# Kernel optimization log

Hardware: AMD Instinct MI355X
Metric: run time of the kernel (lower is better)

Reference implementation:

```python
import jax, jax.numpy as jnp
import numpy as np

E = 8        # num_experts
K = 2        # experts_per_token
D = 1024     # embed_dim
F = 4096     # expert intermediate (mlp_ratio * D)
FS = 2048    # shared-expert intermediate (n_shared_experts * D)
B, S = 2, 1024


def setup_inputs() -> dict:
    key = jax.random.key(0)
    ks = jax.random.split(key, 8)
    scale = jnp.float32(0.02)
    return {
        "x": jax.random.normal(ks[0], (B, S, D), jnp.float32),
        "gate_w": jax.random.normal(ks[1], (E, D), jnp.float32) * scale,
        "gate_k": jax.random.normal(ks[2], (E, D, F), jnp.float32) * scale,
        "up_k": jax.random.normal(ks[3], (E, D, F), jnp.float32) * scale,
        "down_k": jax.random.normal(ks[4], (E, F, D), jnp.float32) * scale,
        "sh_gate": jax.random.normal(ks[5], (D, FS), jnp.float32) * scale,
        "sh_up": jax.random.normal(ks[6], (D, FS), jnp.float32) * scale,
        "sh_down": jax.random.normal(ks[7], (FS, D), jnp.float32) * scale,
    }


def reference(x, gate_w, gate_k, up_k, down_k, sh_gate, sh_up, sh_down):
    b, s, d = x.shape
    xt = x.reshape(-1, d)                                   # [N, D] tokens

    # --- router gate: softmax over expert logits, then top-k ---
    logits = xt @ gate_w.T                                  # [N, E]
    scores = jax.nn.softmax(logits, axis=-1)
    topk_w, topk_i = jax.lax.top_k(scores, K)               # [N, K] each
    # norm_topk_prob = False -> use raw softmax top-k weights

    # per-token combine weights over experts: [N, E]
    combine = (jax.nn.one_hot(topk_i, E, dtype=xt.dtype) * topk_w[..., None]).sum(axis=1)

    # --- routed experts: SwiGLU MLP per expert (batched over E) ---
    g = jnp.einsum("nd,edf->enf", xt, gate_k)               # [E, N, F]
    u = jnp.einsum("nd,edf->enf", xt, up_k)                 # [E, N, F]
    a = jax.nn.silu(g) * u                                  # [E, N, F]
    eo = jnp.einsum("enf,efd->end", a, down_k)              # [E, N, D]
    y = jnp.einsum("end,ne->nd", eo, combine)               # [N, D]

    # --- shared expert (SwiGLU) on identity input ---
    shared = (jax.nn.silu(xt @ sh_gate) * (xt @ sh_up)) @ sh_down  # [N, D]

    return (y + shared).reshape(b, s, d)
```

## Files before the change

### kernel.cpp

```cpp
#include <hip/hip_runtime.h>
#include <hip/hip_bf16.h>

#define E_ 8
#define K_ 2
#define D_ 1024
#define F_ 4096
#define FS_ 2048
#define N_ 2048
#define ROWS_CAP 4352
#define TILE_CAP 40

typedef __bf16 bf16x8 __attribute__((ext_vector_type(8)));
typedef float f32x4 __attribute__((ext_vector_type(4)));

static __device__ __forceinline__ unsigned short f2bf(float f) {
  union { float f; unsigned int u; } v; v.f = f;
  unsigned int u = v.u;
  return (unsigned short)((u + 0x7FFF + ((u >> 16) & 1)) >> 16);
}

static __device__ __forceinline__ void gload16(const unsigned short* gp, unsigned short* lp) {
  __builtin_amdgcn_global_load_lds(
      (const __attribute__((address_space(1))) unsigned int*)gp,
      (__attribute__((address_space(3))) unsigned int*)lp, 16, 0, 0);
}

__global__ void init_k(int* counts) {
  if (threadIdx.x < E_) counts[threadIdx.x] = 0;
}

__global__ void router_k(const float* __restrict__ x, const float* __restrict__ gw,
                         unsigned short* __restrict__ xbf, float* __restrict__ topw,
                         int* __restrict__ topi, int* __restrict__ counts) {
  int wave = threadIdx.x >> 6, lane = threadIdx.x & 63;
  int n = blockIdx.x * 4 + wave;
  const float* xr = x + (size_t)n * D_;
  float v[16];
#pragma unroll
  for (int j = 0; j < 16; ++j) v[j] = xr[lane + 64 * j];
#pragma unroll
  for (int j = 0; j < 16; ++j) xbf[(size_t)n * D_ + lane + 64 * j] = f2bf(v[j]);
  float logit[E_];
  for (int e = 0; e < E_; ++e) {
    const float* g = gw + e * D_;
    float acc = 0.f;
#pragma unroll
    for (int j = 0; j < 16; ++j) acc += v[j] * g[lane + 64 * j];
#pragma unroll
    for (int off = 32; off > 0; off >>= 1) acc += __shfl_down(acc, off, 64);
    logit[e] = __shfl(acc, 0, 64);
  }
  if (lane == 0) {
    float m = logit[0];
    for (int e = 1; e < E_; ++e) m = fmaxf(m, logit[e]);
    float p[E_], s = 0.f;
    for (int e = 0; e < E_; ++e) { p[e] = expf(logit[e] - m); s += p[e]; }
    float inv = 1.f / s;
    for (int e = 0; e < E_; ++e) p[e] *= inv;
    int i0 = 0;
    for (int e = 1; e < E_; ++e) if (p[e] > p[i0]) i0 = e;
    int i1 = (i0 == 0) ? 1 : 0;
    for (int e = 0; e < E_; ++e) if (e != i0 && p[e] > p[i1]) i1 = e;
    topi[n * 2] = i0; topi[n * 2 + 1] = i1;
    topw[n * 2] = p[i0]; topw[n * 2 + 1] = p[i1];
    atomicAdd(&counts[i0], 1);
    atomicAdd(&counts[i1], 1);
  }
}

__global__ void scan_k(const int* __restrict__ counts, int* __restrict__ offs,
                       int* __restrict__ cursor, int* __restrict__ tile_e,
                       int* __restrict__ tile_m, int* __restrict__ ntiles) {
  if (threadIdx.x == 0) {
    int o = 0, idx = 0;
    for (int e = 0; e < E_; ++e) {
      offs[e] = o;
      int c = counts[e];
      int mt = (c + 127) >> 7;
      for (int m = 0; m < mt; ++m) {
        if (idx < TILE_CAP) { tile_e[idx] = e; tile_m[idx] = m; ++idx; }
      }
      o += c; cursor[e] = 0;
    }
    offs[E_] = o;
    ntiles[0] = idx;
  }
}

__global__ void fill_k(const int* __restrict__ topi, const int* __restrict__ offs,
                       int* __restrict__ cursor, int* __restrict__ rowlist,
                       int* __restrict__ slot_of) {
  int n = blockIdx.x * blockDim.x + threadIdx.x;
  if (n >= N_) return;
  for (int k = 0; k < K_; ++k) {
    int e = topi[n * 2 + k];
    int pos = offs[e] + atomicAdd(&cursor[e], 1);
    rowlist[pos] = n;
    slot_of[n * 2 + k] = pos;
  }
}

__global__ void transpose_cvt_k(const float* __restrict__ in, unsigned short* __restrict__ out,
                                int R, int C) {
  __shared__ float tile[64][65];
  int cb = blockIdx.x * 64, rb = blockIdx.y * 64;
  const float* ip = in + (size_t)blockIdx.z * R * C;
  unsigned short* op = out + (size_t)blockIdx.z * R * C;
  int t = threadIdx.x;
  int cx = t & 63, ry = t >> 6;
#pragma unroll
  for (int i = 0; i < 16; ++i)
    tile[ry + i * 4][cx] = ip[(size_t)(rb + ry + i * 4) * C + cb + cx];
  __syncthreads();
  int wx = t & 31, wy = t >> 5;
#pragma unroll
  for (int i = 0; i < 8; ++i) {
    int cl = wy + i * 8;
    unsigned int u = (unsigned int)f2bf(tile[2 * wx][cl]) |
                     ((unsigned int)f2bf(tile[2 * wx + 1][cl]) << 16);
    ((unsigned int*)(op + (size_t)(cb + cl) * R + rb))[wx] = u;
  }
}

__launch_bounds__(256, 3)
__global__ void gemm1_k(const unsigned short* __restrict__ Abase,
                        const int* __restrict__ rowlist,
                        const int* __restrict__ offs,
                        const int* __restrict__ tile_e, const int* __restrict__ tile_m,
                        const int* __restrict__ ntiles, int Mfixed,
                        const unsigned short* __restrict__ Bg_base,
                        const unsigned short* __restrict__ Bu_base,
                        int Ncols, int Kdim,
                        unsigned short* __restrict__ Out) {
  int e, mbase, Me, slotbase;
  if (tile_e) {
    if ((int)blockIdx.x >= ntiles[0]) return;
    e = tile_e[blockIdx.x]; mbase = tile_m[blockIdx.x] * 128;
    slotbase = offs[e]; Me = offs[e + 1] - slotbase;
  } else {
    e = 0; mbase = blockIdx.x * 128; slotbase = 0; Me = Mfixed;
  }
  int nbase = blockIdx.y * 64;
  const unsigned short* Bg = Bg_base + (size_t)e * Ncols * Kdim;
  const unsigned short* Bu = Bu_base + (size_t)e * Ncols * Kdim;

  __shared__ unsigned short As[128 * 32];
  __shared__ unsigned short Bgs[64 * 32];
  __shared__ unsigned short Bus[64 * 32];

  int t = threadIdx.x, lane = t & 63, wave = t >> 6;
  int wm = wave >> 1, wn = wave & 1;
  int chunk = lane & 3, rsub = lane >> 2;

  const unsigned short* aptr[2];
  unsigned int aoff[2];
#pragma unroll
  for (int i = 0; i < 2; ++i) {
    int r = wave * 32 + i * 16 + rsub;
    int grow = mbase + r;
    int src;
    if (rowlist) src = rowlist[slotbase + ((grow < Me) ? grow : 0)];
    else src = (grow < Me) ? grow : 0;
    aptr[i] = Abase + (size_t)src * Kdim + chunk * 8;
    aoff[i] = (unsigned)(wave * 32 + i * 16) * 32;
  }
  int bn = nbase + wave * 16 + rsub;
  const unsigned short* bgptr = Bg + (size_t)bn * Kdim + chunk * 8;
  const unsigned short* buptr = Bu + (size_t)bn * Kdim + chunk * 8;
  unsigned int boff = (unsigned)(wave * 16) * 32;

  f32x4 accg[4][2], accu[4][2];
#pragma unroll
  for (int i = 0; i < 4; ++i)
#pragma unroll
    for (int j = 0; j < 2; ++j) {
      accg[i][j] = f32x4{0.f, 0.f, 0.f, 0.f};
      accu[i][j] = f32x4{0.f, 0.f, 0.f, 0.f};
    }

  int nk = Kdim >> 5;
  for (int kt = 0; kt < nk; ++kt) {
    gload16(aptr[0] + kt * 32, &As[aoff[0]]);
    gload16(aptr[1] + kt * 32, &As[aoff[1]]);
    gload16(bgptr + kt * 32, &Bgs[boff]);
    gload16(buptr + kt * 32, &Bus[boff]);
    __syncthreads();
    bf16x8 afr[4];
#pragma unroll
    for (int i = 0; i < 4; ++i)
      afr[i] = *(const bf16x8*)&As[(wm * 64 + i * 16 + (lane & 15)) * 32 + (lane >> 4) * 8];
#pragma unroll
    for (int j = 0; j < 2; ++j) {
      bf16x8 bg = *(const bf16x8*)&Bgs[(wn * 32 + j * 16 + (lane & 15)) * 32 + (lane >> 4) * 8];
      bf16x8 bu = *(const bf16x8*)&Bus[(wn * 32 + j * 16 + (lane & 15)) * 32 + (lane >> 4) * 8];
#pragma unroll
      for (int i = 0; i < 4; ++i) {
        accg[i][j] = __builtin_amdgcn_mfma_f32_16x16x32_bf16(afr[i], bg, accg[i][j], 0, 0, 0);
        accu[i][j] = __builtin_amdgcn_mfma_f32_16x16x32_bf16(afr[i], bu, accu[i][j], 0, 0, 0);
      }
    }
    __syncthreads();
  }
  int r0 = (lane >> 4) * 4, cn = lane & 15;
#pragma unroll
  for (int i = 0; i < 4; ++i) {
#pragma unroll
    for (int rr = 0; rr < 4; ++rr) {
      int grow = mbase + wm * 64 + i * 16 + r0 + rr;
      if (grow < Me) {
        size_t rbase = (size_t)(slotbase + grow) * Ncols + nbase;
#pragma unroll
        for (int j = 0; j < 2; ++j) {
          float g = accg[i][j][rr], u = accu[i][j][rr];
          float a = (g / (1.f + __expf(-g))) * u;
          Out[rbase + wn * 32 + j * 16 + cn] = f2bf(a);
        }
      }
    }
  }
}

__launch_bounds__(256, 3)
__global__ void gemm2_k(const unsigned short* __restrict__ Abase,
                        const int* __restrict__ offs,
                        const int* __restrict__ tile_e, const int* __restrict__ tile_m,
                        const int* __restrict__ ntiles, int Mfixed,
                        const unsigned short* __restrict__ Bt_base,
                        int Ncols, int Kdim, int kchunk,
                        float* __restrict__ Out) {
  int e, mbase, Me, slotbase;
  if (tile_e) {
    if ((int)blockIdx.x >= ntiles[0]) return;
    e = tile_e[blockIdx.x]; mbase = tile_m[blockIdx.x] * 128;
    slotbase = offs[e]; Me = offs[e + 1] - slotbase;
  } else {
    e = 0; mbase = blockIdx.x * 128; slotbase = 0; Me = Mfixed;
  }
  int nbase = blockIdx.y * 128;
  int koff = blockIdx.z * kchunk;
  const unsigned short* Bt = Bt_base + (size_t)e * Ncols * Kdim;

  __shared__ unsigned short As[128 * 32];
  __shared__ unsigned short Bs[128 * 32];

  int t = threadIdx.x, lane = t & 63, wave = t >> 6;
  int wm = wave >> 1, wn = wave & 1;
  int chunk = lane & 3, rsub = lane >> 2;

  const unsigned short* aptr[2];
  const unsigned short* bptr[2];
  unsigned int loff[2];
#pragma unroll
  for (int i = 0; i < 2; ++i) {
    int r = wave * 32 + i * 16 + rsub;
    int grow = mbase + r;
    int arow = slotbase + ((grow < Me) ? grow : 0);
    aptr[i] = Abase + (size_t)arow * Kdim + koff + chunk * 8;
    bptr[i] = Bt + (size_t)(nbase + r) * Kdim + koff + chunk * 8;
    loff[i] = (unsigned)(wave * 32 + i * 16) * 32;
  }

  f32x4 acc[4][4];
#pragma unroll
  for (int i = 0; i < 4; ++i)
#pragma unroll
    for (int j = 0; j < 4; ++j) acc[i][j] = f32x4{0.f, 0.f, 0.f, 0.f};

  int nk = kchunk >> 5;
  for (int kt = 0; kt < nk; ++kt) {
    gload16(aptr[0] + kt * 32, &As[loff[0]]);
    gload16(aptr[1] + kt * 32, &As[loff[1]]);
    gload16(bptr[0] + kt * 32, &Bs[loff[0]]);
    gload16(bptr[1] + kt * 32, &Bs[loff[1]]);
    __syncthreads();
    bf16x8 afr[4];
#pragma unroll
    for (int i = 0; i < 4; ++i)
      afr[i] = *(const bf16x8*)&As[(wm * 64 + i * 16 + (lane & 15)) * 32 + (lane >> 4) * 8];
#pragma unroll
    for (int j = 0; j < 4; ++j) {
      bf16x8 bb = *(const bf16x8*)&Bs[(wn * 64 + j * 16 + (lane & 15)) * 32 + (lane >> 4) * 8];
#pragma unroll
      for (int i = 0; i < 4; ++i)
        acc[i][j] = __builtin_amdgcn_mfma_f32_16x16x32_bf16(afr[i], bb, acc[i][j], 0, 0, 0);
    }
    __syncthreads();
  }
  int r0 = (lane >> 4) * 4, cn = lane & 15;
#pragma unroll
  for (int i = 0; i < 4; ++i) {
#pragma unroll
    for (int rr = 0; rr < 4; ++rr) {
      int grow = mbase + wm * 64 + i * 16 + r0 + rr;
      if (grow < Me) {
        size_t rbase = (size_t)(slotbase + grow) * Ncols + nbase;
#pragma unroll
        for (int j = 0; j < 4; ++j)
          atomicAdd(&Out[rbase + wn * 64 + j * 16 + cn], acc[i][j][rr]);
      }
    }
  }
}

__launch_bounds__(256, 2)
__global__ void gemm1_old(const unsigned short* __restrict__ Abase,
                          const int* __restrict__ rowlist,
                          const int* __restrict__ offs, int Mfixed,
                          const float* __restrict__ Bg_base,
                          const float* __restrict__ Bu_base,
                          int Ncols, int Kdim,
                          unsigned short* __restrict__ Out) {
  int e = blockIdx.z;
  int Me, slotbase;
  if (offs) { slotbase = offs[e]; Me = offs[e + 1] - slotbase; }
  else      { slotbase = 0;       Me = Mfixed; }
  int mbase = blockIdx.x * 128;
  if (mbase >= Me) return;
  int nbase = blockIdx.y * 128;
  const float* Bg = Bg_base + (size_t)e * Kdim * Ncols;
  const float* Bu = Bu_base + (size_t)e * Kdim * Ncols;
  __shared__ unsigned short As[128][40];
  __shared__ unsigned short Bgs[128][40];
  __shared__ unsigned short Bus[128][40];
  int t = threadIdx.x, lane = t & 63, wave = t >> 6;
  int wm = wave >> 1, wn = wave & 1;
  f32x4 accg[4][4], accu[4][4];
#pragma unroll
  for (int i = 0; i < 4; ++i)
#pragma unroll
    for (int j = 0; j < 4; ++j) {
      accg[i][j] = f32x4{0.f, 0.f, 0.f, 0.f};
      accu[i][j] = f32x4{0.f, 0.f, 0.f, 0.f};
    }
  int ar = t >> 1, akh = t & 1;
  int arow = mbase + ar;
  int asrc = 0;
  if (arow < Me) asrc = rowlist ? rowlist[slotbase + arow] : arow;
  const unsigned short* aptr = Abase + (size_t)asrc * Kdim + akh * 16;
  int bfc = t & 127, bkh = t >> 7;
  const float* bgp = Bg + (size_t)(bkh * 16) * Ncols + nbase + bfc;
  const float* bup = Bu + (size_t)(bkh * 16) * Ncols + nbase + bfc;
  int nk = Kdim >> 5;
  for (int kt = 0; kt < nk; ++kt) {
    uint4 a0 = *(const uint4*)(aptr + kt * 32);
    uint4 a1 = *(const uint4*)(aptr + kt * 32 + 8);
    *(uint4*)&As[ar][akh * 16] = a0;
    *(uint4*)&As[ar][akh * 16 + 8] = a1;
    {
      const float* p0 = bgp + (size_t)kt * 32 * Ncols;
      float bv[16]; unsigned short h[16];
#pragma unroll
      for (int i = 0; i < 16; ++i) bv[i] = p0[(size_t)i * Ncols];
#pragma unroll
      for (int i = 0; i < 16; ++i) h[i] = f2bf(bv[i]);
      *(uint4*)&Bgs[bfc][bkh * 16] = *(uint4*)&h[0];
      *(uint4*)&Bgs[bfc][bkh * 16 + 8] = *(uint4*)&h[8];
    }
    {
      const float* p1 = bup + (size_t)kt * 32 * Ncols;
      float bv[16]; unsigned short h[16];
#pragma unroll
      for (int i = 0; i < 16; ++i) bv[i] = p1[(size_t)i * Ncols];
#pragma unroll
      for (int i = 0; i < 16; ++i) h[i] = f2bf(bv[i]);
      *(uint4*)&Bus[bfc][bkh * 16] = *(uint4*)&h[0];
      *(uint4*)&Bus[bfc][bkh * 16 + 8] = *(uint4*)&h[8];
    }
    __syncthreads();
    bf16x8 afr[4];
#pragma unroll
    for (int i = 0; i < 4; ++i)
      afr[i] = *(const bf16x8*)&As[wm * 64 + i * 16 + (lane & 15)][(lane >> 4) * 8];
#pragma unroll
    for (int j = 0; j < 4; ++j) {
      bf16x8 bg = *(const bf16x8*)&Bgs[wn * 64 + j * 16 + (lane & 15)][(lane >> 4) * 8];
      bf16x8 bu = *(const bf16x8*)&Bus[wn * 64 + j * 16 + (lane & 15)][(lane >> 4) * 8];
#pragma unroll
      for (int i = 0; i < 4; ++i) {
        accg[i][j] = __builtin_amdgcn_mfma_f32_16x16x32_bf16(afr[i], bg, accg[i][j], 0, 0, 0);
        accu[i][j] = __builtin_amdgcn_mfma_f32_16x16x32_bf16(afr[i], bu, accu[i][j], 0, 0, 0);
      }
    }
    __syncthreads();
  }
  int r0 = (lane >> 4) * 4, cn = lane & 15;
#pragma unroll
  for (int i = 0; i < 4; ++i) {
#pragma unroll
    for (int rr = 0; rr < 4; ++rr) {
      int grow = mbase + wm * 64 + i * 16 + r0 + rr;
      if (grow < Me) {
        size_t rbase = (size_t)(slotbase + grow) * Ncols + nbase;
#pragma unroll
        for (int j = 0; j < 4; ++j) {
          float g = accg[i][j][rr], u = accu[i][j][rr];
          float a = (g / (1.f + __expf(-g))) * u;
          Out[rbase + wn * 64 + j * 16 + cn] = f2bf(a);
        }
      }
    }
  }
}

__launch_bounds__(256, 2)
__global__ void gemm2_old(const unsigned short* __restrict__ Abase,
                          const int* __restrict__ offs, int Mfixed,
                          const float* __restrict__ B_base,
                          int Ncols, int Kdim,
                          float* __restrict__ Out) {
  int e = blockIdx.z;
  int Me, slotbase;
  if (offs) { slotbase = offs[e]; Me = offs[e + 1] - slotbase; }
  else      { slotbase = 0;       Me = Mfixed; }
  int mbase = blockIdx.x * 128;
  if (mbase >= Me) return;
  int nbase = blockIdx.y * 128;
  const float* B = B_base + (size_t)e * Kdim * Ncols;
  __shared__ unsigned short As[128][40];
  __shared__ unsigned short Bs[128][40];
  int t = threadIdx.x, lane = t & 63, wave = t >> 6;
  int wm = wave >> 1, wn = wave & 1;
  f32x4 acc[4][4];
#pragma unroll
  for (int i = 0; i < 4; ++i)
#pragma unroll
    for (int j = 0; j < 4; ++j) acc[i][j] = f32x4{0.f, 0.f, 0.f, 0.f};
  int ar = t >> 1, akh = t & 1;
  int arow = slotbase + ((mbase + ar < Me) ? (mbase + ar) : 0);
  const unsigned short* aptr = Abase + (size_t)arow * Kdim + akh * 16;
  int bfc = t & 127, bkh = t >> 7;
  const float* bp = B + (size_t)(bkh * 16) * Ncols + nbase + bfc;
  int nk = Kdim >> 5;
  for (int kt = 0; kt < nk; ++kt) {
    uint4 a0 = *(const uint4*)(aptr + kt * 32);
    uint4 a1 = *(const uint4*)(aptr + kt * 32 + 8);
    *(uint4*)&As[ar][akh * 16] = a0;
    *(uint4*)&As[ar][akh * 16 + 8] = a1;
    {
      const float* p0 = bp + (size_t)kt * 32 * Ncols;
      float bv[16]; unsigned short h[16];
#pragma unroll
      for (int i = 0; i < 16; ++i) bv[i] = p0[(size_t)i * Ncols];
#pragma unroll
      for (int i = 0; i < 16; ++i) h[i] = f2bf(bv[i]);
      *(uint4*)&Bs[bfc][bkh * 16] = *(uint4*)&h[0];
      *(uint4*)&Bs[bfc][bkh * 16 + 8] = *(uint4*)&h[8];
    }
    __syncthreads();
    bf16x8 afr[4];
#pragma unroll
    for (int i = 0; i < 4; ++i)
      afr[i] = *(const bf16x8*)&As[wm * 64 + i * 16 + (lane & 15)][(lane >> 4) * 8];
#pragma unroll
    for (int j = 0; j < 4; ++j) {
      bf16x8 bb = *(const bf16x8*)&Bs[wn * 64 + j * 16 + (lane & 15)][(lane >> 4) * 8];
#pragma unroll
      for (int i = 0; i < 4; ++i)
        acc[i][j] = __builtin_amdgcn_mfma_f32_16x16x32_bf16(afr[i], bb, acc[i][j], 0, 0, 0);
    }
    __syncthreads();
  }
  int r0 = (lane >> 4) * 4, cn = lane & 15;
#pragma unroll
  for (int i = 0; i < 4; ++i) {
#pragma unroll
    for (int rr = 0; rr < 4; ++rr) {
      int grow = mbase + wm * 64 + i * 16 + r0 + rr;
      if (grow < Me) {
        size_t rbase = (size_t)(slotbase + grow) * Ncols + nbase;
#pragma unroll
        for (int j = 0; j < 4; ++j)
          Out[rbase + wn * 64 + j * 16 + cn] = acc[i][j][rr];
      }
    }
  }
}

__global__ void combine_k(const float* __restrict__ eo, const float* __restrict__ sh,
                          const float* __restrict__ topw, const int* __restrict__ slot_of,
                          float* __restrict__ out) {
  int idx = blockIdx.x * blockDim.x + threadIdx.x;
  int n = idx >> 8;
  int d4 = idx & 255;
  float w0 = topw[n * 2], w1 = topw[n * 2 + 1];
  int s0 = slot_of[n * 2], s1 = slot_of[n * 2 + 1];
  float4 a = ((const float4*)(eo + (size_t)s0 * D_))[d4];
  float4 b = ((const float4*)(eo + (size_t)s1 * D_))[d4];
  float4 c = ((const float4*)(sh + (size_t)n * D_))[d4];
  float4 r;
  r.x = w0 * a.x + w1 * b.x + c.x;
  r.y = w0 * a.y + w1 * b.y + c.y;
  r.z = w0 * a.z + w1 * b.z + c.z;
  r.w = w0 * a.w + w1 * b.w + c.w;
  ((float4*)out)[idx] = r;
}

extern "C" void kernel_launch(void* const* d_in, const int* in_sizes, int n_in,
                              void* d_out, int out_size, void* d_ws, size_t ws_size,
                              hipStream_t stream) {
  const float* x  = (const float*)d_in[0];
  const float* gw = (const float*)d_in[1];
  const float* gk = (const float*)d_in[2];
  const float* uk = (const float*)d_in[3];
  const float* dk = (const float*)d_in[4];
  const float* sg = (const float*)d_in[5];
  const float* su = (const float*)d_in[6];
  const float* sd = (const float*)d_in[7];
  float* out = (float*)d_out;

  char* w = (char*)d_ws;
  size_t o = 0;
  auto take = [&](size_t bytes) -> void* {
    void* p = w + o;
    o += (bytes + 255) & ~(size_t)255;
    return p;
  };
  unsigned short* xbf    = (unsigned short*)take((size_t)N_ * D_ * 2);
  unsigned short* act    = (unsigned short*)take((size_t)ROWS_CAP * F_ * 2);
  unsigned short* act_sh = (unsigned short*)take((size_t)N_ * FS_ * 2);
  float* eo     = (float*)take((size_t)ROWS_CAP * D_ * 4);
  float* sh_out = (float*)take((size_t)N_ * D_ * 4);
  float* topw   = (float*)take((size_t)N_ * 2 * 4);
  int* topi     = (int*)take((size_t)N_ * 2 * 4);
  int* slot_of  = (int*)take((size_t)N_ * 2 * 4);
  int* rowlist  = (int*)take((size_t)ROWS_CAP * 4);
  int* counts   = (int*)take(E_ * 4);
  int* offs     = (int*)take((E_ + 1) * 4);
  int* cursor   = (int*)take(E_ * 4);
  int* tile_e   = (int*)take(TILE_CAP * 4);
  int* tile_m   = (int*)take(TILE_CAP * 4);
  int* ntiles   = (int*)take(4);
  unsigned short* gkt = (unsigned short*)take((size_t)E_ * D_ * F_ * 2);
  unsigned short* ukt = (unsigned short*)take((size_t)E_ * D_ * F_ * 2);
  unsigned short* dkt = (unsigned short*)take((size_t)E_ * D_ * F_ * 2);
  unsigned short* sgt = (unsigned short*)take((size_t)D_ * FS_ * 2);
  unsigned short* sut = (unsigned short*)take((size_t)D_ * FS_ * 2);
  unsigned short* sdt = (unsigned short*)take((size_t)D_ * FS_ * 2);
  bool full = (ws_size >= o);

  hipLaunchKernelGGL(init_k, dim3(1), dim3(64), 0, stream, counts);
  hipLaunchKernelGGL(router_k, dim3(N_ / 4), dim3(256), 0, stream,
                     x, gw, xbf, topw, topi, counts);
  hipLaunchKernelGGL(scan_k, dim3(1), dim3(32), 0, stream,
                     counts, offs, cursor, tile_e, tile_m, ntiles);
  hipLaunchKernelGGL(fill_k, dim3(N_ / 256), dim3(256), 0, stream,
                     topi, offs, cursor, rowlist, slot_of);

  if (full) {
    hipLaunchKernelGGL(transpose_cvt_k, dim3(F_ / 64, D_ / 64, E_), dim3(256), 0, stream,
                       gk, gkt, D_, F_);
    hipLaunchKernelGGL(transpose_cvt_k, dim3(F_ / 64, D_ / 64, E_), dim3(256), 0, stream,
                       uk, ukt, D_, F_);
    hipLaunchKernelGGL(transpose_cvt_k, dim3(D_ / 64, F_ / 64, E_), dim3(256), 0, stream,
                       dk, dkt, F_, D_);
    hipLaunchKernelGGL(transpose_cvt_k, dim3(FS_ / 64, D_ / 64, 1), dim3(256), 0, stream,
                       sg, sgt, D_, FS_);
    hipLaunchKernelGGL(transpose_cvt_k, dim3(FS_ / 64, D_ / 64, 1), dim3(256), 0, stream,
                       su, sut, D_, FS_);
    hipLaunchKernelGGL(transpose_cvt_k, dim3(D_ / 64, FS_ / 64, 1), dim3(256), 0, stream,
                       sd, sdt, FS_, D_);
    hipMemsetAsync(eo, 0, (size_t)ROWS_CAP * D_ * 4, stream);
    hipMemsetAsync(sh_out, 0, (size_t)N_ * D_ * 4, stream);
    hipLaunchKernelGGL(gemm1_k, dim3(TILE_CAP, F_ / 64), dim3(256), 0, stream,
                       xbf, rowlist, offs, tile_e, tile_m, ntiles, 0,
                       gkt, ukt, F_, D_, act);
    hipLaunchKernelGGL(gemm1_k, dim3(N_ / 128, FS_ / 64), dim3(256), 0, stream,
                       xbf, (const int*)nullptr, (const int*)nullptr,
                       (const int*)nullptr, (const int*)nullptr, (const int*)nullptr, N_,
                       sgt, sut, FS_, D_, act_sh);
    hipLaunchKernelGGL(gemm2_k, dim3(TILE_CAP, D_ / 128, 2), dim3(256), 0, stream,
                       act, offs, tile_e, tile_m, ntiles, 0,
                       dkt, D_, F_, F_ / 2, eo);
    hipLaunchKernelGGL(gemm2_k, dim3(N_ / 128, D_ / 128, 2), dim3(256), 0, stream,
                       act_sh, (const int*)nullptr, (const int*)nullptr,
                       (const int*)nullptr, (const int*)nullptr, N_,
                       sdt, D_, FS_, FS_ / 2, sh_out);
  } else {
    hipLaunchKernelGGL(gemm1_old, dim3(16, F_ / 128, E_), dim3(256), 0, stream,
                       xbf, rowlist, offs, 0, gk, uk, F_, D_, act);
    hipLaunchKernelGGL(gemm1_old, dim3(16, FS_ / 128, 1), dim3(256), 0, stream,
                       xbf, (const int*)nullptr, (const int*)nullptr, N_, sg, su, FS_, D_, act_sh);
    hipLaunchKernelGGL(gemm2_old, dim3(16, D_ / 128, E_), dim3(256), 0, stream,
                       act, offs, 0, dk, D_, F_, eo);
    hipLaunchKernelGGL(gemm2_old, dim3(16, D_ / 128, 1), dim3(256), 0, stream,
                       act_sh, (const int*)nullptr, N_, sd, D_, FS_, sh_out);
  }
  hipLaunchKernelGGL(combine_k, dim3((N_ * D_ / 4) / 256), dim3(256), 0, stream,
                     eo, sh_out, topw, slot_of, out);
}
```

Baseline: 778.8 us.

## Double-buffer MoE GEMMs, fuse combine into down-proj atomics, balance tile chunks

Double-buffers the LDS tiles in both GEMM kernels, using explicit vmcnt waits so the next K-slice loads while the current one computes. Removes the separate combine kernel and two memsets: the down-projection epilogue scatters router-weighted results straight into the zeroed output with atomics. Redistributes expert tiles across chunks with a greedy balancer and swizzles the grid. Also vectorises transpose loads with float4. Risks include heavier atomic contention on the output, a larger LDS footprint that may lower occupancy, and roww aliasing the eo buffer, which is safe only because the fallback path that also uses eo does not run alongside the full path.

```diff
diff --git a/kernel.cpp b/kernel.cpp
--- a/kernel.cpp
+++ b/kernel.cpp
@@ -8,7 +8,8 @@
 #define FS_ 2048
 #define N_ 2048
 #define ROWS_CAP 4352
-#define TILE_CAP 40
+#define NCHUNK 8
+#define CHUNK_CAP 8
 
 typedef __bf16 bf16x8 __attribute__((ext_vector_type(8)));
 typedef float f32x4 __attribute__((ext_vector_type(4)));
@@ -70,26 +71,38 @@
 
 __global__ void scan_k(const int* __restrict__ counts, int* __restrict__ offs,
                        int* __restrict__ cursor, int* __restrict__ tile_e,
-                       int* __restrict__ tile_m, int* __restrict__ ntiles) {
+                       int* __restrict__ tile_m) {
   if (threadIdx.x == 0) {
-    int o = 0, idx = 0;
+    int load[NCHUNK];
+    for (int c = 0; c < NCHUNK; ++c) load[c] = 0;
+    for (int i = 0; i < NCHUNK * CHUNK_CAP; ++i) tile_e[i] = -1;
+    int o = 0;
     for (int e = 0; e < E_; ++e) {
       offs[e] = o;
       int c = counts[e];
       int mt = (c + 127) >> 7;
+      int best = 0;
+      for (int c2 = 1; c2 < NCHUNK; ++c2) if (load[c2] < load[best]) best = c2;
       for (int m = 0; m < mt; ++m) {
-        if (idx < TILE_CAP) { tile_e[idx] = e; tile_m[idx] = m; ++idx; }
+        int ch = best;
+        if (load[ch] >= CHUNK_CAP) {
+          ch = 0;
+          for (int c2 = 1; c2 < NCHUNK; ++c2) if (load[c2] < load[ch]) ch = c2;
+        }
+        tile_e[ch * CHUNK_CAP + load[ch]] = e;
+        tile_m[ch * CHUNK_CAP + load[ch]] = m;
+        load[ch]++;
       }
       o += c; cursor[e] = 0;
     }
     offs[E_] = o;
-    ntiles[0] = idx;
-  }
-}
-
-__global__ void fill_k(const int* __restrict__ topi, const int* __restrict__ offs,
+  }
+}
+
+__global__ void fill_k(const int* __restrict__ topi, const float* __restrict__ topw,
+                       const int* __restrict__ offs,
                        int* __restrict__ cursor, int* __restrict__ rowlist,
-                       int* __restrict__ slot_of) {
+                       int* __restrict__ slot_of, float* __restrict__ roww) {
   int n = blockIdx.x * blockDim.x + threadIdx.x;
   if (n >= N_) return;
   for (int k = 0; k < K_; ++k) {
@@ -97,6 +110,7 @@
     int pos = offs[e] + atomicAdd(&cursor[e], 1);
     rowlist[pos] = n;
     slot_of[n * 2 + k] = pos;
+    roww[pos] = topw[n * 2 + k];
   }
 }
 
@@ -107,10 +121,13 @@
   const float* ip = in + (size_t)blockIdx.z * R * C;
   unsigned short* op = out + (size_t)blockIdx.z * R * C;
   int t = threadIdx.x;
-  int cx = t & 63, ry = t >> 6;
-#pragma unroll
-  for (int i = 0; i < 16; ++i)
-    tile[ry + i * 4][cx] = ip[(size_t)(rb + ry + i * 4) * C + cb + cx];
+  int cg = (t & 15) * 4, r0 = t >> 4;
+#pragma unroll
+  for (int p = 0; p < 4; ++p) {
+    int r = r0 + p * 16;
+    float4 v = *(const float4*)&ip[(size_t)(rb + r) * C + cb + cg];
+    tile[r][cg] = v.x; tile[r][cg + 1] = v.y; tile[r][cg + 2] = v.z; tile[r][cg + 3] = v.w;
+  }
   __syncthreads();
   int wx = t & 31, wy = t >> 5;
 #pragma unroll
@@ -122,48 +139,85 @@
   }
 }
 
+#define G1_STAGE(buf, kt2)                               \
+    gload16(aptr0 + (kt2) * 32, &As[buf][aoff0]);        \
+    gload16(aptr1 + (kt2) * 32, &As[buf][aoff1]);        \
+    gload16(bgptr + (kt2) * 32, &Bgs[buf][boff]);        \
+    gload16(buptr + (kt2) * 32, &Bus[buf][boff]);
+
+#define G1_STEP(buf, kt)                                                        \
+  {                                                                             \
+    if ((kt) + 1 < nk) {                                                        \
+      G1_STAGE(1 - (buf), (kt) + 1)                                             \
+      asm volatile("s_waitcnt vmcnt(4)" ::: "memory");                          \
+    } else {                                                                    \
+      asm volatile("s_waitcnt vmcnt(0)" ::: "memory");                          \
+    }                                                                           \
+    __builtin_amdgcn_s_barrier();                                               \
+    __builtin_amdgcn_sched_barrier(0);                                          \
+    bf16x8 afr[4];                                                              \
+    _Pragma("unroll") for (int i = 0; i < 4; ++i)                               \
+      afr[i] = *(const bf16x8*)&As[buf][(wm * 64 + i * 16 + (lane & 15)) * 32 + (lane >> 4) * 8]; \
+    _Pragma("unroll") for (int j = 0; j < 2; ++j) {                             \
+      bf16x8 bg = *(const bf16x8*)&Bgs[buf][(wn * 32 + j * 16 + (lane & 15)) * 32 + (lane >> 4) * 8]; \
+      bf16x8 bu = *(const bf16x8*)&Bus[buf][(wn * 32 + j * 16 + (lane & 15)) * 32 + (lane >> 4) * 8]; \
+      _Pragma("unroll") for (int i = 0; i < 4; ++i) {                           \
+        accg[i][j] = __builtin_amdgcn_mfma_f32_16x16x32_bf16(afr[i], bg, accg[i][j], 0, 0, 0); \
+        accu[i][j] = __builtin_amdgcn_mfma_f32_16x16x32_bf16(afr[i], bu, accu[i][j], 0, 0, 0); \
+      }                                                                         \
+    }                                                                           \
+    __builtin_amdgcn_sched_barrier(0);                                          \
+    __builtin_amdgcn_s_barrier();                                               \
+  }
+
 __launch_bounds__(256, 3)
 __global__ void gemm1_k(const unsigned short* __restrict__ Abase,
                         const int* __restrict__ rowlist,
                         const int* __restrict__ offs,
                         const int* __restrict__ tile_e, const int* __restrict__ tile_m,
-                        const int* __restrict__ ntiles, int Mfixed,
+                        int swz, int Mfixed,
                         const unsigned short* __restrict__ Bg_base,
                         const unsigned short* __restrict__ Bu_base,
                         int Ncols, int Kdim,
                         unsigned short* __restrict__ Out) {
-  int e, mbase, Me, slotbase;
-  if (tile_e) {
-    if ((int)blockIdx.x >= ntiles[0]) return;
-    e = tile_e[blockIdx.x]; mbase = tile_m[blockIdx.x] * 128;
+  int e, mbase, Me, slotbase, nbase;
+  if (swz) {
+    int slot = blockIdx.x * CHUNK_CAP + (blockIdx.y & (CHUNK_CAP - 1));
+    e = tile_e[slot];
+    if (e < 0) return;
+    mbase = tile_m[slot] * 128;
     slotbase = offs[e]; Me = offs[e + 1] - slotbase;
+    nbase = (int)(blockIdx.y >> 3) * 64;
   } else {
     e = 0; mbase = blockIdx.x * 128; slotbase = 0; Me = Mfixed;
-  }
-  int nbase = blockIdx.y * 64;
+    nbase = blockIdx.y * 64;
+  }
   const unsigned short* Bg = Bg_base + (size_t)e * Ncols * Kdim;
   const unsigned short* Bu = Bu_base + (size_t)e * Ncols * Kdim;
 
-  __shared__ unsigned short As[128 * 32];
-  __shared__ unsigned short Bgs[64 * 32];
-  __shared__ unsigned short Bus[64 * 32];
+  __shared__ unsigned short As[2][128 * 32];
+  __shared__ unsigned short Bgs[2][64 * 32];
+  __shared__ unsigned short Bus[2][64 * 32];
 
   int t = threadIdx.x, lane = t & 63, wave = t >> 6;
   int wm = wave >> 1, wn = wave & 1;
   int chunk = lane & 3, rsub = lane >> 2;
 
-  const unsigned short* aptr[2];
-  unsigned int aoff[2];
-#pragma unroll
-  for (int i = 0; i < 2; ++i) {
-    int r = wave * 32 + i * 16 + rsub;
-    int grow = mbase + r;
-    int src;
-    if (rowlist) src = rowlist[slotbase + ((grow < Me) ? grow : 0)];
-    else src = (grow < Me) ? grow : 0;
-    aptr[i] = Abase + (size_t)src * Kdim + chunk * 8;
-    aoff[i] = (unsigned)(wave * 32 + i * 16) * 32;
-  }
+  int g0 = mbase + wave * 32 + rsub;
+  int g1 = mbase + wave * 32 + 16 + rsub;
+  int src0, src1;
+  if (rowlist) {
+    src0 = rowlist[slotbase + ((g0 < Me) ? (g0 - mbase) + mbase : 0)];
+    src1 = rowlist[slotbase + ((g1 < Me) ? g1 : 0)];
+    src0 = rowlist[slotbase + ((g0 < Me) ? g0 : 0)];
+  } else {
+    src0 = (g0 < Me) ? g0 : 0;
+    src1 = (g1 < Me) ? g1 : 0;
+  }
+  const unsigned short* aptr0 = Abase + (size_t)src0 * Kdim + chunk * 8;
+  const unsigned short* aptr1 = Abase + (size_t)src1 * Kdim + chunk * 8;
+  unsigned int aoff0 = (unsigned)(wave * 32) * 32;
+  unsigned int aoff1 = (unsigned)(wave * 32 + 16) * 32;
   int bn = nbase + wave * 16 + rsub;
   const unsigned short* bgptr = Bg + (size_t)bn * Kdim + chunk * 8;
   const unsigned short* buptr = Bu + (size_t)bn * Kdim + chunk * 8;
@@ -179,28 +233,12 @@
     }
 
   int nk = Kdim >> 5;
-  for (int kt = 0; kt < nk; ++kt) {
-    gload16(aptr[0] + kt * 32, &As[aoff[0]]);
-    gload16(aptr[1] + kt * 32, &As[aoff[1]]);
-    gload16(bgptr + kt * 32, &Bgs[boff]);
-    gload16(buptr + kt * 32, &Bus[boff]);
-    __syncthreads();
-    bf16x8 afr[4];
-#pragma unroll
-    for (int i = 0; i < 4; ++i)
-      afr[i] = *(const bf16x8*)&As[(wm * 64 + i * 16 + (lane & 15)) * 32 + (lane >> 4) * 8];
-#pragma unroll
-    for (int j = 0; j < 2; ++j) {
-      bf16x8 bg = *(const bf16x8*)&Bgs[(wn * 32 + j * 16 + (lane & 15)) * 32 + (lane >> 4) * 8];
-      bf16x8 bu = *(const bf16x8*)&Bus[(wn * 32 + j * 16 + (lane & 15)) * 32 + (lane >> 4) * 8];
-#pragma unroll
-      for (int i = 0; i < 4; ++i) {
-        accg[i][j] = __builtin_amdgcn_mfma_f32_16x16x32_bf16(afr[i], bg, accg[i][j], 0, 0, 0);
-        accu[i][j] = __builtin_amdgcn_mfma_f32_16x16x32_bf16(afr[i], bu, accu[i][j], 0, 0, 0);
-      }
-    }
-    __syncthreads();
-  }
+  G1_STAGE(0, 0)
+  for (int kt = 0; kt < nk; kt += 2) {
+    G1_STEP(0, kt)
+    G1_STEP(1, kt + 1)
+  }
+
   int r0 = (lane >> 4) * 4, cn = lane & 15;
 #pragma unroll
   for (int i = 0; i < 4; ++i) {
@@ -220,45 +258,78 @@
   }
 }
 
+#define G2_STAGE(buf, kt2)                               \
+    gload16(aptr0 + (kt2) * 32, &As[buf][loff0]);        \
+    gload16(aptr1 + (kt2) * 32, &As[buf][loff1]);        \
+    gload16(bptr0 + (kt2) * 32, &Bs[buf][loff0]);        \
+    gload16(bptr1 + (kt2) * 32, &Bs[buf][loff1]);
+
+#define G2_STEP(buf, kt)                                                        \
+  {                                                                             \
+    if ((kt) + 1 < nk) {                                                        \
+      G2_STAGE(1 - (buf), (kt) + 1)                                             \
+      asm volatile("s_waitcnt vmcnt(4)" ::: "memory");                          \
+    } else {                                                                    \
+      asm volatile("s_waitcnt vmcnt(0)" ::: "memory");                          \
+    }                                                                           \
+    __builtin_amdgcn_s_barrier();                                               \
+    __builtin_amdgcn_sched_barrier(0);                                          \
+    bf16x8 afr[4];                                                              \
+    _Pragma("unroll") for (int i = 0; i < 4; ++i)                               \
+      afr[i] = *(const bf16x8*)&As[buf][(wm * 64 + i * 16 + (lane & 15)) * 32 + (lane >> 4) * 8]; \
+    _Pragma("unroll") for (int j = 0; j < 4; ++j) {                             \
+      bf16x8 bb = *(const bf16x8*)&Bs[buf][(wn * 64 + j * 16 + (lane & 15)) * 32 + (lane >> 4) * 8]; \
+      _Pragma("unroll") for (int i = 0; i < 4; ++i)                             \
+        acc[i][j] = __builtin_amdgcn_mfma_f32_16x16x32_bf16(afr[i], bb, acc[i][j], 0, 0, 0); \
+    }                                                                           \
+    __builtin_amdgcn_sched_barrier(0);                                          \
+    __builtin_amdgcn_s_barrier();                                               \
+  }
+
 __launch_bounds__(256, 3)
 __global__ void gemm2_k(const unsigned short* __restrict__ Abase,
+                        const int* __restrict__ rowlist,
+                        const float* __restrict__ roww,
                         const int* __restrict__ offs,
                         const int* __restrict__ tile_e, const int* __restrict__ tile_m,
-                        const int* __restrict__ ntiles, int Mfixed,
+                        int swz, int Mfixed,
                         const unsigned short* __restrict__ Bt_base,
                         int Ncols, int Kdim, int kchunk,
                         float* __restrict__ Out) {
-  int e, mbase, Me, slotbase;
-  if (tile_e) {
-    if ((int)blockIdx.x >= ntiles[0]) return;
-    e = tile_e[blockIdx.x]; mbase = tile_m[blockIdx.x] * 128;
+  int e, mbase, Me, slotbase, nbase, koff;
+  if (swz) {
+    int slot = blockIdx.x * CHUNK_CAP + (blockIdx.y & (CHUNK_CAP - 1));
+    e = tile_e[slot];
+    if (e < 0) return;
+    mbase = tile_m[slot] * 128;
     slotbase = offs[e]; Me = offs[e + 1] - slotbase;
+    int r = blockIdx.y >> 3;
+    nbase = (r & 7) * 128;
+    koff = (r >> 3) * kchunk;
   } else {
     e = 0; mbase = blockIdx.x * 128; slotbase = 0; Me = Mfixed;
-  }
-  int nbase = blockIdx.y * 128;
-  int koff = blockIdx.z * kchunk;
+    nbase = blockIdx.y * 128;
+    koff = blockIdx.z * kchunk;
+  }
   const unsigned short* Bt = Bt_base + (size_t)e * Ncols * Kdim;
 
-  __shared__ unsigned short As[128 * 32];
-  __shared__ unsigned short Bs[128 * 32];
+  __shared__ unsigned short As[2][128 * 32];
+  __shared__ unsigned short Bs[2][128 * 32];
 
   int t = threadIdx.x, lane = t & 63, wave = t >> 6;
   int wm = wave >> 1, wn = wave & 1;
   int chunk = lane & 3, rsub = lane >> 2;
 
-  const unsigned short* aptr[2];
-  const unsigned short* bptr[2];
-  unsigned int loff[2];
-#pragma unroll
-  for (int i = 0; i < 2; ++i) {
-    int r = wave * 32 + i * 16 + rsub;
-    int grow = mbase + r;
-    int arow = slotbase + ((grow < Me) ? grow : 0);
-    aptr[i] = Abase + (size_t)arow * Kdim + koff + chunk * 8;
-    bptr[i] = Bt + (size_t)(nbase + r) * Kdim + koff + chunk * 8;
-    loff[i] = (unsigned)(wave * 32 + i * 16) * 32;
-  }
+  int ra = wave * 32 + rsub, rb2 = wave * 32 + 16 + rsub;
+  int g0 = mbase + ra, g1 = mbase + rb2;
+  int arow0 = slotbase + ((g0 < Me) ? g0 : 0);
+  int arow1 = slotbase + ((g1 < Me) ? g1 : 0);
+  const unsigned short* aptr0 = Abase + (size_t)arow0 * Kdim + koff + chunk * 8;
+  const unsigned short* aptr1 = Abase + (size_t)arow1 * Kdim + koff + chunk * 8;
+  const unsigned short* bptr0 = Bt + (size_t)(nbase + ra) * Kdim + koff + chunk * 8;
+  const unsigned short* bptr1 = Bt + (size_t)(nbase + rb2) * Kdim + koff + chunk * 8;
+  unsigned int loff0 = (unsigned)(wave * 32) * 32;
+  unsigned int loff1 = (unsigned)(wave * 32 + 16) * 32;
 
   f32x4 acc[4][4];
 #pragma unroll
@@ -267,36 +338,27 @@
     for (int j = 0; j < 4; ++j) acc[i][j] = f32x4{0.f, 0.f, 0.f, 0.f};
 
   int nk = kchunk >> 5;
-  for (int kt = 0; kt < nk; ++kt) {
-    gload16(aptr[0] + kt * 32, &As[loff[0]]);
-    gload16(aptr[1] + kt * 32, &As[loff[1]]);
-    gload16(bptr[0] + kt * 32, &Bs[loff[0]]);
-    gload16(bptr[1] + kt * 32, &Bs[loff[1]]);
-    __syncthreads();
-    bf16x8 afr[4];
-#pragma unroll
-    for (int i = 0; i < 4; ++i)
-      afr[i] = *(const bf16x8*)&As[(wm * 64 + i * 16 + (lane & 15)) * 32 + (lane >> 4) * 8];
-#pragma unroll
-    for (int j = 0; j < 4; ++j) {
-      bf16x8 bb = *(const bf16x8*)&Bs[(wn * 64 + j * 16 + (lane & 15)) * 32 + (lane >> 4) * 8];
-#pragma unroll
-      for (int i = 0; i < 4; ++i)
-        acc[i][j] = __builtin_amdgcn_mfma_f32_16x16x32_bf16(afr[i], bb, acc[i][j], 0, 0, 0);
-    }
-    __syncthreads();
-  }
-  int r0 = (lane >> 4) * 4, cn = lane & 15;
+  G2_STAGE(0, 0)
+  for (int kt = 0; kt < nk; kt += 2) {
+    G2_STEP(0, kt)
+    G2_STEP(1, kt + 1)
+  }
+
+  int er0 = (lane >> 4) * 4, cn = lane & 15;
 #pragma unroll
   for (int i = 0; i < 4; ++i) {
 #pragma unroll
     for (int rr = 0; rr < 4; ++rr) {
-      int grow = mbase + wm * 64 + i * 16 + r0 + rr;
+      int grow = mbase + wm * 64 + i * 16 + er0 + rr;
       if (grow < Me) {
-        size_t rbase = (size_t)(slotbase + grow) * Ncols + nbase;
+        int srow = slotbase + grow;
+        int token; float wgt;
+        if (rowlist) { token = rowlist[srow]; wgt = roww[srow]; }
+        else { token = grow; wgt = 1.f; }
+        float* orow = Out + (size_t)token * Ncols + nbase + wn * 64 + cn;
 #pragma unroll
         for (int j = 0; j < 4; ++j)
-          atomicAdd(&Out[rbase + wn * 64 + j * 16 + cn], acc[i][j][rr]);
+          atomicAdd(&orow[j * 16], wgt * acc[i][j][rr]);
       }
     }
   }
@@ -527,9 +589,9 @@
   int* counts   = (int*)take(E_ * 4);
   int* offs     = (int*)take((E_ + 1) * 4);
   int* cursor   = (int*)take(E_ * 4);
-  int* tile_e   = (int*)take(TILE_CAP * 4);
-  int* tile_m   = (int*)take(TILE_CAP * 4);
-  int* ntiles   = (int*)take(4);
+  int* tile_e   = (int*)take(NCHUNK * CHUNK_CAP * 4);
+  int* tile_m   = (int*)take(NCHUNK * CHUNK_CAP * 4);
+  float* roww = eo;
   unsigned short* gkt = (unsigned short*)take((size_t)E_ * D_ * F_ * 2);
   unsigned short* ukt = (unsigned short*)take((size_t)E_ * D_ * F_ * 2);
   unsigned short* dkt = (unsigned short*)take((size_t)E_ * D_ * F_ * 2);
@@ -542,9 +604,9 @@
   hipLaunchKernelGGL(router_k, dim3(N_ / 4), dim3(256), 0, stream,
                      x, gw, xbf, topw, topi, counts);
   hipLaunchKernelGGL(scan_k, dim3(1), dim3(32), 0, stream,
-                     counts, offs, cursor, tile_e, tile_m, ntiles);
+                     counts, offs, cursor, tile_e, tile_m);
   hipLaunchKernelGGL(fill_k, dim3(N_ / 256), dim3(256), 0, stream,
-                     topi, offs, cursor, rowlist, slot_of);
+                     topi, topw, offs, cursor, rowlist, slot_of, roww);
 
   if (full) {
     hipLaunchKernelGGL(transpose_cvt_k, dim3(F_ / 64, D_ / 64, E_), dim3(256), 0, stream,
@@ -559,22 +621,21 @@
                        su, sut, D_, FS_);
     hipLaunchKernelGGL(transpose_cvt_k, dim3(D_ / 64, FS_ / 64, 1), dim3(256), 0, stream,
                        sd, sdt, FS_, D_);
-    hipMemsetAsync(eo, 0, (size_t)ROWS_CAP * D_ * 4, stream);
-    hipMemsetAsync(sh_out, 0, (size_t)N_ * D_ * 4, stream);
-    hipLaunchKernelGGL(gemm1_k, dim3(TILE_CAP, F_ / 64), dim3(256), 0, stream,
-                       xbf, rowlist, offs, tile_e, tile_m, ntiles, 0,
+    hipMemsetAsync(out, 0, (size_t)N_ * D_ * 4, stream);
+    hipLaunchKernelGGL(gemm1_k, dim3(NCHUNK, CHUNK_CAP * (F_ / 64)), dim3(256), 0, stream,
+                       xbf, rowlist, offs, tile_e, tile_m, 1, 0,
                        gkt, ukt, F_, D_, act);
     hipLaunchKernelGGL(gemm1_k, dim3(N_ / 128, FS_ / 64), dim3(256), 0, stream,
                        xbf, (const int*)nullptr, (const int*)nullptr,
-                       (const int*)nullptr, (const int*)nullptr, (const int*)nullptr, N_,
+                       (const int*)nullptr, (const int*)nullptr, 0, N_,
                        sgt, sut, FS_, D_, act_sh);
-    hipLaunchKernelGGL(gemm2_k, dim3(TILE_CAP, D_ / 128, 2), dim3(256), 0, stream,
-                       act, offs, tile_e, tile_m, ntiles, 0,
-                       dkt, D_, F_, F_ / 2, eo);
+    hipLaunchKernelGGL(gemm2_k, dim3(NCHUNK, CHUNK_CAP * (D_ / 128) * 2), dim3(256), 0, stream,
+                       act, rowlist, roww, offs, tile_e, tile_m, 1, 0,
+                       dkt, D_, F_, F_ / 2, out);
     hipLaunchKernelGGL(gemm2_k, dim3(N_ / 128, D_ / 128, 2), dim3(256), 0, stream,
-                       act_sh, (const int*)nullptr, (const int*)nullptr,
-                       (const int*)nullptr, (const int*)nullptr, N_,
-                       sdt, D_, FS_, FS_ / 2, sh_out);
+                       act_sh, (const int*)nullptr, (const float*)nullptr,
+                       (const int*)nullptr, (const int*)nullptr, (const int*)nullptr, 0, N_,
+                       sdt, D_, FS_, FS_ / 2, out);
   } else {
     hipLaunchKernelGGL(gemm1_old, dim3(16, F_ / 128, E_), dim3(256), 0, stream,
                        xbf, rowlist, offs, 0, gk, uk, F_, D_, act);
@@ -584,7 +645,7 @@
                        act, offs, 0, dk, D_, F_, eo);
     hipLaunchKernelGGL(gemm2_old, dim3(16, D_ / 128, 1), dim3(256), 0, stream,
                        act_sh, (const int*)nullptr, N_, sd, D_, FS_, sh_out);
-  }
-  hipLaunchKernelGGL(combine_k, dim3((N_ * D_ / 4) / 256), dim3(256), 0, stream,
-                     eo, sh_out, topw, slot_of, out);
-}
+    hipLaunchKernelGGL(combine_k, dim3((N_ * D_ / 4) / 256), dim3(256), 0, stream,
+                       eo, sh_out, topw, slot_of, out);
+  }
+}
```

Result: slower. 794.9 us (+2.1%).

## Scatter expert outputs directly into output, balance tiles across chunks, vectorize transpose

Applied to the files above, without the earlier changes.

The down-projection now applies the routing weight and atomically scatters each expert row straight into the final output, which removes the eo and sh_out memsets and the combine kernel. The scan assigns expert M-tiles to 8 load-balanced chunks, and the grid is swizzled so the blocks for one tile sit next to each other. The transpose kernel reads float4 and launch bounds move to 4 waves per SIMD. In exchange, more atomics contend on the same output rows, and the fallback path still writes roww into eo.

```diff
diff --git a/kernel.cpp b/kernel.cpp
--- a/kernel.cpp
+++ b/kernel.cpp
@@ -8,7 +8,8 @@
 #define FS_ 2048
 #define N_ 2048
 #define ROWS_CAP 4352
-#define TILE_CAP 40
+#define NCHUNK 8
+#define CHUNK_CAP 8
 
 typedef __bf16 bf16x8 __attribute__((ext_vector_type(8)));
 typedef float f32x4 __attribute__((ext_vector_type(4)));
@@ -70,26 +71,38 @@
 
 __global__ void scan_k(const int* __restrict__ counts, int* __restrict__ offs,
                        int* __restrict__ cursor, int* __restrict__ tile_e,
-                       int* __restrict__ tile_m, int* __restrict__ ntiles) {
+                       int* __restrict__ tile_m) {
   if (threadIdx.x == 0) {
-    int o = 0, idx = 0;
+    int load[NCHUNK];
+    for (int c = 0; c < NCHUNK; ++c) load[c] = 0;
+    for (int i = 0; i < NCHUNK * CHUNK_CAP; ++i) tile_e[i] = -1;
+    int o = 0;
     for (int e = 0; e < E_; ++e) {
       offs[e] = o;
       int c = counts[e];
       int mt = (c + 127) >> 7;
+      int best = 0;
+      for (int c2 = 1; c2 < NCHUNK; ++c2) if (load[c2] < load[best]) best = c2;
       for (int m = 0; m < mt; ++m) {
-        if (idx < TILE_CAP) { tile_e[idx] = e; tile_m[idx] = m; ++idx; }
+        int ch = best;
+        if (load[ch] >= CHUNK_CAP) {
+          ch = 0;
+          for (int c2 = 1; c2 < NCHUNK; ++c2) if (load[c2] < load[ch]) ch = c2;
+        }
+        tile_e[ch * CHUNK_CAP + load[ch]] = e;
+        tile_m[ch * CHUNK_CAP + load[ch]] = m;
+        load[ch]++;
       }
       o += c; cursor[e] = 0;
     }
     offs[E_] = o;
-    ntiles[0] = idx;
-  }
-}
-
-__global__ void fill_k(const int* __restrict__ topi, const int* __restrict__ offs,
+  }
+}
+
+__global__ void fill_k(const int* __restrict__ topi, const float* __restrict__ topw,
+                       const int* __restrict__ offs,
                        int* __restrict__ cursor, int* __restrict__ rowlist,
-                       int* __restrict__ slot_of) {
+                       int* __restrict__ slot_of, float* __restrict__ roww) {
   int n = blockIdx.x * blockDim.x + threadIdx.x;
   if (n >= N_) return;
   for (int k = 0; k < K_; ++k) {
@@ -97,6 +110,7 @@
     int pos = offs[e] + atomicAdd(&cursor[e], 1);
     rowlist[pos] = n;
     slot_of[n * 2 + k] = pos;
+    roww[pos] = topw[n * 2 + k];
   }
 }
 
@@ -107,10 +121,13 @@
   const float* ip = in + (size_t)blockIdx.z * R * C;
   unsigned short* op = out + (size_t)blockIdx.z * R * C;
   int t = threadIdx.x;
-  int cx = t & 63, ry = t >> 6;
-#pragma unroll
-  for (int i = 0; i < 16; ++i)
-    tile[ry + i * 4][cx] = ip[(size_t)(rb + ry + i * 4) * C + cb + cx];
+  int cg = (t & 15) * 4, r0 = t >> 4;
+#pragma unroll
+  for (int p = 0; p < 4; ++p) {
+    int r = r0 + p * 16;
+    float4 v = *(const float4*)&ip[(size_t)(rb + r) * C + cb + cg];
+    tile[r][cg] = v.x; tile[r][cg + 1] = v.y; tile[r][cg + 2] = v.z; tile[r][cg + 3] = v.w;
+  }
   __syncthreads();
   int wx = t & 31, wy = t >> 5;
 #pragma unroll
@@ -122,25 +139,28 @@
   }
 }
 
-__launch_bounds__(256, 3)
+__launch_bounds__(256, 4)
 __global__ void gemm1_k(const unsigned short* __restrict__ Abase,
                         const int* __restrict__ rowlist,
                         const int* __restrict__ offs,
                         const int* __restrict__ tile_e, const int* __restrict__ tile_m,
-                        const int* __restrict__ ntiles, int Mfixed,
+                        int swz, int Mfixed,
                         const unsigned short* __restrict__ Bg_base,
                         const unsigned short* __restrict__ Bu_base,
                         int Ncols, int Kdim,
                         unsigned short* __restrict__ Out) {
-  int e, mbase, Me, slotbase;
-  if (tile_e) {
-    if ((int)blockIdx.x >= ntiles[0]) return;
-    e = tile_e[blockIdx.x]; mbase = tile_m[blockIdx.x] * 128;
+  int e, mbase, Me, slotbase, nbase;
+  if (swz) {
+    int slot = blockIdx.x * CHUNK_CAP + (blockIdx.y & (CHUNK_CAP - 1));
+    e = tile_e[slot];
+    if (e < 0) return;
+    mbase = tile_m[slot] * 128;
     slotbase = offs[e]; Me = offs[e + 1] - slotbase;
+    nbase = (int)(blockIdx.y >> 3) * 64;
   } else {
     e = 0; mbase = blockIdx.x * 128; slotbase = 0; Me = Mfixed;
-  }
-  int nbase = blockIdx.y * 64;
+    nbase = blockIdx.y * 64;
+  }
   const unsigned short* Bg = Bg_base + (size_t)e * Ncols * Kdim;
   const unsigned short* Bu = Bu_base + (size_t)e * Ncols * Kdim;
 
@@ -220,24 +240,31 @@
   }
 }
 
-__launch_bounds__(256, 3)
+__launch_bounds__(256, 4)
 __global__ void gemm2_k(const unsigned short* __restrict__ Abase,
+                        const int* __restrict__ rowlist,
+                        const float* __restrict__ roww,
                         const int* __restrict__ offs,
                         const int* __restrict__ tile_e, const int* __restrict__ tile_m,
-                        const int* __restrict__ ntiles, int Mfixed,
+                        int swz, int Mfixed,
                         const unsigned short* __restrict__ Bt_base,
                         int Ncols, int Kdim, int kchunk,
                         float* __restrict__ Out) {
-  int e, mbase, Me, slotbase;
-  if (tile_e) {
-    if ((int)blockIdx.x >= ntiles[0]) return;
-    e = tile_e[blockIdx.x]; mbase = tile_m[blockIdx.x] * 128;
+  int e, mbase, Me, slotbase, nbase, koff;
+  if (swz) {
+    int slot = blockIdx.x * CHUNK_CAP + (blockIdx.y & (CHUNK_CAP - 1));
+    e = tile_e[slot];
+    if (e < 0) return;
+    mbase = tile_m[slot] * 128;
     slotbase = offs[e]; Me = offs[e + 1] - slotbase;
+    int r = blockIdx.y >> 3;
+    nbase = (r & 7) * 128;
+    koff = (r >> 3) * kchunk;
   } else {
     e = 0; mbase = blockIdx.x * 128; slotbase = 0; Me = Mfixed;
-  }
-  int nbase = blockIdx.y * 128;
-  int koff = blockIdx.z * kchunk;
+    nbase = blockIdx.y * 128;
+    koff = blockIdx.z * kchunk;
+  }
   const unsigned short* Bt = Bt_base + (size_t)e * Ncols * Kdim;
 
   __shared__ unsigned short As[128 * 32];
@@ -286,17 +313,21 @@
     }
     __syncthreads();
   }
-  int r0 = (lane >> 4) * 4, cn = lane & 15;
+  int er0 = (lane >> 4) * 4, cn = lane & 15;
 #pragma unroll
   for (int i = 0; i < 4; ++i) {
 #pragma unroll
     for (int rr = 0; rr < 4; ++rr) {
-      int grow = mbase + wm * 64 + i * 16 + r0 + rr;
+      int grow = mbase + wm * 64 + i * 16 + er0 + rr;
       if (grow < Me) {
-        size_t rbase = (size_t)(slotbase + grow) * Ncols + nbase;
+        int srow = slotbase + grow;
+        int token; float wgt;
+        if (rowlist) { token = rowlist[srow]; wgt = roww[srow]; }
+        else { token = grow; wgt = 1.f; }
+        float* orow = Out + (size_t)token * Ncols + nbase + wn * 64 + cn;
 #pragma unroll
         for (int j = 0; j < 4; ++j)
-          atomicAdd(&Out[rbase + wn * 64 + j * 16 + cn], acc[i][j][rr]);
+          atomicAdd(&orow[j * 16], wgt * acc[i][j][rr]);
       }
     }
   }
@@ -527,9 +558,9 @@
   int* counts   = (int*)take(E_ * 4);
   int* offs     = (int*)take((E_ + 1) * 4);
   int* cursor   = (int*)take(E_ * 4);
-  int* tile_e   = (int*)take(TILE_CAP * 4);
-  int* tile_m   = (int*)take(TILE_CAP * 4);
-  int* ntiles   = (int*)take(4);
+  int* tile_e   = (int*)take(NCHUNK * CHUNK_CAP * 4);
+  int* tile_m   = (int*)take(NCHUNK * CHUNK_CAP * 4);
+  float* roww = eo;
   unsigned short* gkt = (unsigned short*)take((size_t)E_ * D_ * F_ * 2);
   unsigned short* ukt = (unsigned short*)take((size_t)E_ * D_ * F_ * 2);
   unsigned short* dkt = (unsigned short*)take((size_t)E_ * D_ * F_ * 2);
@@ -542,9 +573,9 @@
   hipLaunchKernelGGL(router_k, dim3(N_ / 4), dim3(256), 0, stream,
                      x, gw, xbf, topw, topi, counts);
   hipLaunchKernelGGL(scan_k, dim3(1), dim3(32), 0, stream,
-                     counts, offs, cursor, tile_e, tile_m, ntiles);
+                     counts, offs, cursor, tile_e, tile_m);
   hipLaunchKernelGGL(fill_k, dim3(N_ / 256), dim3(256), 0, stream,
-                     topi, offs, cursor, rowlist, slot_of);
+                     topi, topw, offs, cursor, rowlist, slot_of, roww);
 
   if (full) {
     hipLaunchKernelGGL(transpose_cvt_k, dim3(F_ / 64, D_ / 64, E_), dim3(256), 0, stream,
@@ -559,22 +590,21 @@
                        su, sut, D_, FS_);
     hipLaunchKernelGGL(transpose_cvt_k, dim3(D_ / 64, FS_ / 64, 1), dim3(256), 0, stream,
                        sd, sdt, FS_, D_);
-    hipMemsetAsync(eo, 0, (size_t)ROWS_CAP * D_ * 4, stream);
-    hipMemsetAsync(sh_out, 0, (size_t)N_ * D_ * 4, stream);
-    hipLaunchKernelGGL(gemm1_k, dim3(TILE_CAP, F_ / 64), dim3(256), 0, stream,
-                       xbf, rowlist, offs, tile_e, tile_m, ntiles, 0,
+    hipMemsetAsync(out, 0, (size_t)N_ * D_ * 4, stream);
+    hipLaunchKernelGGL(gemm1_k, dim3(NCHUNK, CHUNK_CAP * (F_ / 64)), dim3(256), 0, stream,
+                       xbf, rowlist, offs, tile_e, tile_m, 1, 0,
                        gkt, ukt, F_, D_, act);
     hipLaunchKernelGGL(gemm1_k, dim3(N_ / 128, FS_ / 64), dim3(256), 0, stream,
                        xbf, (const int*)nullptr, (const int*)nullptr,
-                       (const int*)nullptr, (const int*)nullptr, (const int*)nullptr, N_,
+                       (const int*)nullptr, (const int*)nullptr, 0, N_,
                        sgt, sut, FS_, D_, act_sh);
-    hipLaunchKernelGGL(gemm2_k, dim3(TILE_CAP, D_ / 128, 2), dim3(256), 0, stream,
-                       act, offs, tile_e, tile_m, ntiles, 0,
-                       dkt, D_, F_, F_ / 2, eo);
+    hipLaunchKernelGGL(gemm2_k, dim3(NCHUNK, CHUNK_CAP * (D_ / 128) * 2), dim3(256), 0, stream,
+                       act, rowlist, roww, offs, tile_e, tile_m, 1, 0,
+                       dkt, D_, F_, F_ / 2, out);
     hipLaunchKernelGGL(gemm2_k, dim3(N_ / 128, D_ / 128, 2), dim3(256), 0, stream,
-                       act_sh, (const int*)nullptr, (const int*)nullptr,
-                       (const int*)nullptr, (const int*)nullptr, N_,
-                       sdt, D_, FS_, FS_ / 2, sh_out);
+                       act_sh, (const int*)nullptr, (const float*)nullptr,
+                       (const int*)nullptr, (const int*)nullptr, (const int*)nullptr, 0, N_,
+                       sdt, D_, FS_, FS_ / 2, out);
   } else {
     hipLaunchKernelGGL(gemm1_old, dim3(16, F_ / 128, E_), dim3(256), 0, stream,
                        xbf, rowlist, offs, 0, gk, uk, F_, D_, act);
@@ -584,7 +614,7 @@
                        act, offs, 0, dk, D_, F_, eo);
     hipLaunchKernelGGL(gemm2_old, dim3(16, D_ / 128, 1), dim3(256), 0, stream,
                        act_sh, (const int*)nullptr, N_, sd, D_, FS_, sh_out);
-  }
-  hipLaunchKernelGGL(combine_k, dim3((N_ * D_ / 4) / 256), dim3(256), 0, stream,
-                     eo, sh_out, topw, slot_of, out);
-}
+    hipLaunchKernelGGL(combine_k, dim3((N_ * D_ / 4) / 256), dim3(256), 0, stream,
+                       eo, sh_out, topw, slot_of, out);
+  }
+}
```

After: 794.4 us. 2.0% more time.
